# Performance work log

Hardware: AMD Instinct MI355X
Metric: run time of the kernel (lower is better)

Reference implementation:

```python
import jax, jax.numpy as jnp
import numpy as np

DIM = 1024
FFN = 4096
E = 10      # num_domains
N = 8192    # tokens
STEPS = 1   # GatedMLP steps (depth=1 layer)


def gated_mlp(x, W1, b1, W2, b2, Wg, bg):
    # depth=1, steps=STEPS; dropout=0 (eval). Residual MLP block with sigmoid gate.
    h = x
    for _ in range(STEPS):
        h = jax.nn.gelu(h @ W1 + b1, approximate=False) @ W2 + b2 + h
    g = jax.nn.sigmoid(x @ Wg + bg)
    return g * h + (1.0 - g) * x


def setup_inputs() -> dict:
    key = jax.random.key(0)
    ks = jax.random.split(key, 16)
    s1 = 1.0 / np.sqrt(DIM)
    s2 = 1.0 / np.sqrt(FFN)
    inp = {
        "x": jax.random.normal(ks[0], (N, DIM), dtype=jnp.float32),
        "domain_ids": jax.random.randint(ks[1], (N,), 0, E, dtype=jnp.int32),
        # shared expert
        "sW1": jax.random.normal(ks[2], (DIM, FFN), dtype=jnp.float32) * s1,
        "sb1": jnp.zeros((FFN,), dtype=jnp.float32),
        "sW2": jax.random.normal(ks[3], (FFN, DIM), dtype=jnp.float32) * s2,
        "sb2": jnp.zeros((DIM,), dtype=jnp.float32),
        "sWg": jax.random.normal(ks[4], (DIM, DIM), dtype=jnp.float32) * (0.01 * s1),
        "sbg": jnp.full((DIM,), -4.0, dtype=jnp.float32),
        # domain experts, stacked over E
        "dW1": jax.random.normal(ks[5], (E, DIM, FFN), dtype=jnp.float32) * s1,
        "db1": jnp.zeros((E, FFN), dtype=jnp.float32),
        "dW2": jax.random.normal(ks[6], (E, FFN, DIM), dtype=jnp.float32) * s2,
        "db2": jnp.zeros((E, DIM), dtype=jnp.float32),
        "dWg": jax.random.normal(ks[7], (E, DIM, DIM), dtype=jnp.float32) * (0.01 * s1),
        "dbg": jnp.full((E, DIM), -4.0, dtype=jnp.float32),
    }
    return inp


def reference(x, domain_ids, sW1, sb1, sW2, sb2, sWg, sbg,
              dW1, db1, dW2, db2, dWg, dbg):
    out = gated_mlp(x, sW1, sb1, sW2, sb2, sWg, sbg)
    # each token belongs to exactly one domain expert; dense dispatch via mask
    for e in range(E):
        mask = (domain_ids == e).astype(x.dtype)[:, None]  # [N,1]
        expert_out = gated_mlp(x, dW1[e], db1[e], dW2[e], db2[e], dWg[e], dbg[e])
        out = out + mask * expert_out
    return out
```

## Files before the change

### kernel.cpp

```cpp
#include <hip/hip_runtime.h>
#include <hip/hip_bf16.h>
#include <math.h>

#define NTOK 8192
#define DIM  1024
#define FFN  4096
#define NEXP 10

#define NT_SH (NTOK / 128)
#define NT_RT (NTOK / 128 + NEXP - 1)
#define NY01  ((FFN + DIM) / 128)
#define NY2   (DIM / 128)

typedef __attribute__((ext_vector_type(8))) short bf16x8;
typedef __attribute__((ext_vector_type(4))) float f32x4;

static __device__ __forceinline__ unsigned short f2bf(float f) {
  __hip_bfloat16 h = __float2bfloat16(f);
  return *reinterpret_cast<unsigned short*>(&h);
}

static __device__ __forceinline__ void gld_lds16(const unsigned short* g, unsigned short* l) {
  __builtin_amdgcn_global_load_lds((const __attribute__((address_space(1))) unsigned int*)g,
                                   (__attribute__((address_space(3))) unsigned int*)l,
                                   16, 0, 0);
}

template <int NX, int NY, int G>
static __device__ __forceinline__ void map_block(int orig, int& bx, int& by) {
  const int n = NX * NY;
  int xcd = orig & 7, o = orig >> 3;
  const int q = n >> 3, r = n & 7;
  int id = (xcd < r ? xcd * (q + 1) : r * (q + 1) + (xcd - r) * q) + o;
  const int gsz = NX * G;
  int grp = id / gsz;
  int rem = id - grp * gsz;
  bx = rem / G;
  by = grp * G + (rem - bx * G);
}

__global__ void k_zero(int* cnt) { if (threadIdx.x < NEXP) cnt[threadIdx.x] = 0; }

__global__ void k_count(const int* __restrict__ dom, int* __restrict__ cnt, int* __restrict__ pos) {
  int t = blockIdx.x * 256 + threadIdx.x;
  if (t < NTOK) pos[t] = atomicAdd(&cnt[dom[t]], 1);
}

__global__ void k_offsets(const int* __restrict__ cnt, int* __restrict__ segoff,
                          int* __restrict__ tilemap, int* __restrict__ ntiles) {
  if (threadIdx.x == 0) {
    int s = 0, k = 0;
    for (int e = 0; e < NEXP; e++) {
      segoff[e] = s;
      int c = cnt[e];
      int nt = (c + 127) >> 7;
      for (int t = 0; t < nt; t++) tilemap[k++] = (e << 16) | t;
      s += c;
    }
    segoff[NEXP] = s;
    *ntiles = k;
  }
}

__global__ void k_scatter(const int* __restrict__ dom, const int* __restrict__ pos,
                          const int* __restrict__ segoff, int* __restrict__ perm) {
  int t = blockIdx.x * 256 + threadIdx.x;
  if (t < NTOK) perm[segoff[dom[t]] + pos[t]] = t;
}

__global__ void k_convert(const float* __restrict__ src, unsigned short* __restrict__ dst, int n8) {
  int i = blockIdx.x * 256 + threadIdx.x;
  if (i >= n8) return;
  const float4* s = (const float4*)(src + (size_t)i * 8);
  float4 a = s[0], b = s[1];
  union { unsigned short h[8]; uint4 v; } u;
  u.h[0] = f2bf(a.x); u.h[1] = f2bf(a.y); u.h[2] = f2bf(a.z); u.h[3] = f2bf(a.w);
  u.h[4] = f2bf(b.x); u.h[5] = f2bf(b.y); u.h[6] = f2bf(b.z); u.h[7] = f2bf(b.w);
  *(uint4*)(dst + (size_t)i * 8) = u.v;
}

__global__ void k_gather(const unsigned short* __restrict__ xb, const int* __restrict__ perm,
                         unsigned short* __restrict__ xs) {
  int i = blockIdx.x * 256 + threadIdx.x;
  int row = i >> 7;
  int c = (i & 127) * 8;
  int src = perm[row];
  *(uint4*)(xs + (size_t)row * DIM + c) = *(const uint4*)(xb + (size_t)src * DIM + c);
}

__global__ void k_transpose(const float* __restrict__ src, unsigned short* __restrict__ dst,
                            int K, int N) {
  size_t moff = (size_t)blockIdx.z * K * N;
  src += moff; dst += moff;
  __shared__ float tile[64][65];
  int n0 = blockIdx.x * 64, k0 = blockIdx.y * 64;
  int t = threadIdx.x;
  int tx = t & 15, ty = t >> 4;
#pragma unroll
  for (int i = 0; i < 4; i++) {
    int kk = ty + i * 16;
    float4 v = *(const float4*)(src + (size_t)(k0 + kk) * N + n0 + tx * 4);
    tile[kk][tx * 4 + 0] = v.x; tile[kk][tx * 4 + 1] = v.y;
    tile[kk][tx * 4 + 2] = v.z; tile[kk][tx * 4 + 3] = v.w;
  }
  __syncthreads();
#pragma unroll
  for (int i = 0; i < 2; i++) {
    int chunk = t + i * 256;
    int nl = chunk >> 3;
    int k8 = (chunk & 7) * 8;
    union { unsigned short h[8]; uint4 v; } u;
#pragma unroll
    for (int j = 0; j < 8; j++) u.h[j] = f2bf(tile[k8 + j][nl]);
    *(uint4*)(dst + (size_t)(n0 + nl) * K + k0 + k8) = u.v;
  }
}

static __device__ __forceinline__ void mfma_tile(
    const unsigned short* gA0, const unsigned short* gA1,
    const unsigned short* gB0, const unsigned short* gB1,
    unsigned short (*As)[32], unsigned short (*Bs)[32],
    int w, int lane, int K, f32x4 acc[4][4])
{
  unsigned short* lA0 = &As[0][0] + w * 1024;
  unsigned short* lA1 = lA0 + 512;
  unsigned short* lB0 = &Bs[0][0] + w * 1024;
  unsigned short* lB1 = lB0 + 512;
  int m16 = lane & 15, kh = (lane >> 4) * 8;
  int wr = (w >> 1) * 64, wc = (w & 1) * 64;
  for (int kt = 0; kt < K; kt += 32) {
    gld_lds16(gA0, lA0); gld_lds16(gA1, lA1);
    gld_lds16(gB0, lB0); gld_lds16(gB1, lB1);
    gA0 += 32; gA1 += 32; gB0 += 32; gB1 += 32;
    __syncthreads();
    bf16x8 af[4], bfr[4];
#pragma unroll
    for (int i = 0; i < 4; i++) af[i] = *(const bf16x8*)&As[wr + i * 16 + m16][kh];
#pragma unroll
    for (int j = 0; j < 4; j++) bfr[j] = *(const bf16x8*)&Bs[wc + j * 16 + m16][kh];
#pragma unroll
    for (int i = 0; i < 4; i++)
#pragma unroll
      for (int j = 0; j < 4; j++)
        acc[i][j] = __builtin_amdgcn_mfma_f32_16x16x32_bf16(af[i], bfr[j], acc[i][j], 0, 0, 0);
    __syncthreads();
  }
}

template <bool ROUTED>
__global__ __launch_bounds__(256)
void k_gemm01(const unsigned short* __restrict__ A,
              const unsigned short* __restrict__ W1t,
              const float* __restrict__ b1,
              const unsigned short* __restrict__ Wgt,
              const float* __restrict__ bg,
              unsigned short* __restrict__ h1,
              float* __restrict__ g,
              const int* __restrict__ segoff,
              const int* __restrict__ tilemap,
              const int* __restrict__ ntilesp) {
  constexpr int NX = ROUTED ? NT_RT : NT_SH;
  int bx, by;
  map_block<NX, NY01, 8>((int)blockIdx.x, bx, by);

  int e = 0, seg0 = 0, cnt = NTOK, m0;
  if (ROUTED) {
    if (bx >= *ntilesp) return;
    int tm = tilemap[bx];
    e = tm >> 16;
    seg0 = segoff[e];
    cnt = segoff[e + 1] - seg0;
    m0 = (tm & 0xffff) << 7;
  } else {
    m0 = bx << 7;
  }

  const bool isW1 = by < (FFN / 128);
  const int n0 = (isW1 ? by : by - FFN / 128) << 7;
  const unsigned short* Bte = isW1 ? W1t + (size_t)e * FFN * DIM + (size_t)n0 * DIM
                                   : Wgt + (size_t)e * DIM * DIM + (size_t)n0 * DIM;
  const float* be = (isW1 ? b1 + (size_t)e * FFN : bg + (size_t)e * DIM) + n0;

  __shared__ unsigned short As[128][32];
  __shared__ unsigned short Bs[128][32];

  int tid = threadIdx.x, w = tid >> 6, lane = tid & 63;
  int p0 = w * 128 + lane;
  int r0 = p0 >> 2, r1 = r0 + 16;
  int kc = (p0 & 3) * 8;

  auto arow = [&](int rl) -> size_t {
    int l = m0 + rl;
    if (ROUTED && l > cnt - 1) l = cnt - 1;
    return (size_t)(seg0 + l);
  };
  const unsigned short* gA0 = A + arow(r0) * DIM + kc;
  const unsigned short* gA1 = A + arow(r1) * DIM + kc;
  const unsigned short* gB0 = Bte + (size_t)r0 * DIM + kc;
  const unsigned short* gB1 = Bte + (size_t)r1 * DIM + kc;

  f32x4 acc[4][4];
#pragma unroll
  for (int i = 0; i < 4; i++)
#pragma unroll
    for (int j = 0; j < 4; j++) acc[i][j] = (f32x4){0.f, 0.f, 0.f, 0.f};

  mfma_tile(gA0, gA1, gB0, gB1, As, Bs, w, lane, DIM, acc);

  int m16 = lane & 15, quad = lane >> 4;
  int wr = (w >> 1) * 64, wc = (w & 1) * 64;
#pragma unroll
  for (int i = 0; i < 4; i++) {
#pragma unroll
    for (int j = 0; j < 4; j++) {
      int cn = wc + j * 16 + m16;
      int col = n0 + cn;
#pragma unroll
      for (int r = 0; r < 4; r++) {
        int rl = wr + i * 16 + quad * 4 + r;
        int l = m0 + rl;
        if (ROUTED && l >= cnt) continue;
        float z = acc[i][j][r] + be[cn];
        size_t row = (size_t)(seg0 + l);
        if (isW1) {
          z = 0.5f * z * (1.0f + erff(z * 0.70710678118654752f));
          h1[row * FFN + col] = f2bf(z);
        } else {
          z = 1.0f / (1.0f + expf(-z));
          g[row * DIM + col] = z;
        }
      }
    }
  }
}

template <bool ROUTED>
__global__ __launch_bounds__(256)
void k_gemm2(const unsigned short* __restrict__ A,
             const unsigned short* __restrict__ W2t,
             const float* __restrict__ b2,
             const float* __restrict__ g,
             const float* __restrict__ xres,
             float* __restrict__ out,
             const int* __restrict__ perm,
             const int* __restrict__ segoff,
             const int* __restrict__ tilemap,
             const int* __restrict__ ntilesp) {
  constexpr int NX = ROUTED ? NT_RT : NT_SH;
  int bx, by;
  map_block<NX, NY2, 2>((int)blockIdx.x, bx, by);

  int e = 0, seg0 = 0, cnt = NTOK, m0;
  if (ROUTED) {
    if (bx >= *ntilesp) return;
    int tm = tilemap[bx];
    e = tm >> 16;
    seg0 = segoff[e];
    cnt = segoff[e + 1] - seg0;
    m0 = (tm & 0xffff) << 7;
  } else {
    m0 = bx << 7;
  }
  const int n0 = by << 7;
  const unsigned short* Bte = W2t + (size_t)e * DIM * FFN + (size_t)n0 * FFN;
  const float* be = b2 + (size_t)e * DIM + n0;

  __shared__ unsigned short As[128][32];
  __shared__ unsigned short Bs[128][32];

  int tid = threadIdx.x, w = tid >> 6, lane = tid & 63;
  int p0 = w * 128 + lane;
  int r0 = p0 >> 2, r1 = r0 + 16;
  int kc = (p0 & 3) * 8;

  auto arow = [&](int rl) -> size_t {
    int l = m0 + rl;
    if (ROUTED && l > cnt - 1) l = cnt - 1;
    return (size_t)(seg0 + l);
  };
  const unsigned short* gA0 = A + arow(r0) * FFN + kc;
  const unsigned short* gA1 = A + arow(r1) * FFN + kc;
  const unsigned short* gB0 = Bte + (size_t)r0 * FFN + kc;
  const unsigned short* gB1 = Bte + (size_t)r1 * FFN + kc;

  f32x4 acc[4][4];
#pragma unroll
  for (int i = 0; i < 4; i++)
#pragma unroll
    for (int j = 0; j < 4; j++) acc[i][j] = (f32x4){0.f, 0.f, 0.f, 0.f};

  mfma_tile(gA0, gA1, gB0, gB1, As, Bs, w, lane, FFN, acc);

  int m16 = lane & 15, quad = lane >> 4;
  int wr = (w >> 1) * 64, wc = (w & 1) * 64;
#pragma unroll
  for (int i = 0; i < 4; i++) {
#pragma unroll
    for (int j = 0; j < 4; j++) {
      int cn = wc + j * 16 + m16;
      int col = n0 + cn;
#pragma unroll
      for (int r = 0; r < 4; r++) {
        int rl = wr + i * 16 + quad * 4 + r;
        int l = m0 + rl;
        if (ROUTED && l >= cnt) continue;
        int lidx = seg0 + l;
        int grow = ROUTED ? perm[lidx] : l;
        float xv = xres[(size_t)grow * DIM + col];
        float gv = g[(size_t)lidx * DIM + col];
        float h = acc[i][j][r] + be[cn] + xv;
        float o = gv * h + (1.0f - gv) * xv;
        float* po = &out[(size_t)grow * DIM + col];
        if (ROUTED) *po += o;
        else        *po = o;
      }
    }
  }
}

extern "C" void kernel_launch(void* const* d_in, const int* in_sizes, int n_in,
                              void* d_out, int out_size, void* d_ws, size_t ws_size,
                              hipStream_t stream) {
  (void)in_sizes; (void)n_in; (void)out_size; (void)ws_size;
  const float* x   = (const float*)d_in[0];
  const int*   dom = (const int*)d_in[1];
  const float* sW1 = (const float*)d_in[2];
  const float* sb1 = (const float*)d_in[3];
  const float* sW2 = (const float*)d_in[4];
  const float* sb2 = (const float*)d_in[5];
  const float* sWg = (const float*)d_in[6];
  const float* sbg = (const float*)d_in[7];
  const float* dW1 = (const float*)d_in[8];
  const float* db1 = (const float*)d_in[9];
  const float* dW2 = (const float*)d_in[10];
  const float* db2 = (const float*)d_in[11];
  const float* dWg = (const float*)d_in[12];
  const float* dbg = (const float*)d_in[13];
  float* out = (float*)d_out;

  char* p = (char*)d_ws;
  auto take = [&](size_t b) { char* r = p; p += (b + 255) & ~(size_t)255; return r; };
  int* cnt     = (int*)take(NEXP * 4);
  int* segoff  = (int*)take((NEXP + 1) * 4);
  int* tilemap = (int*)take(128 * 4);
  int* ntiles  = (int*)take(4);
  int* pos     = (int*)take((size_t)NTOK * 4);
  int* perm    = (int*)take((size_t)NTOK * 4);
  unsigned short* xb   = (unsigned short*)take((size_t)NTOK * DIM * 2);
  unsigned short* xs   = (unsigned short*)take((size_t)NTOK * DIM * 2);
  unsigned short* h1   = (unsigned short*)take((size_t)NTOK * FFN * 2);
  float*          g    = (float*)take((size_t)NTOK * DIM * 4);
  unsigned short* sW1t = (unsigned short*)take((size_t)DIM * FFN * 2);
  unsigned short* sW2t = (unsigned short*)take((size_t)FFN * DIM * 2);
  unsigned short* sWgt = (unsigned short*)take((size_t)DIM * DIM * 2);
  unsigned short* dW1t = (unsigned short*)take((size_t)NEXP * DIM * FFN * 2);
  unsigned short* dW2t = (unsigned short*)take((size_t)NEXP * FFN * DIM * 2);
  unsigned short* dWgt = (unsigned short*)take((size_t)NEXP * DIM * DIM * 2);

  k_zero<<<1, 64, 0, stream>>>(cnt);
  k_count<<<NTOK / 256, 256, 0, stream>>>(dom, cnt, pos);
  k_offsets<<<1, 1, 0, stream>>>(cnt, segoff, tilemap, ntiles);
  k_scatter<<<NTOK / 256, 256, 0, stream>>>(dom, pos, segoff, perm);

  k_convert<<<(NTOK * DIM / 8) / 256, 256, 0, stream>>>(x, xb, NTOK * DIM / 8);
  k_gather<<<(NTOK * DIM / 8) / 256, 256, 0, stream>>>(xb, perm, xs);
  k_transpose<<<dim3(FFN / 64, DIM / 64, 1),    256, 0, stream>>>(sW1, sW1t, DIM, FFN);
  k_transpose<<<dim3(DIM / 64, FFN / 64, 1),    256, 0, stream>>>(sW2, sW2t, FFN, DIM);
  k_transpose<<<dim3(DIM / 64, DIM / 64, 1),    256, 0, stream>>>(sWg, sWgt, DIM, DIM);
  k_transpose<<<dim3(FFN / 64, DIM / 64, NEXP), 256, 0, stream>>>(dW1, dW1t, DIM, FFN);
  k_transpose<<<dim3(DIM / 64, FFN / 64, NEXP), 256, 0, stream>>>(dW2, dW2t, FFN, DIM);
  k_transpose<<<dim3(DIM / 64, DIM / 64, NEXP), 256, 0, stream>>>(dWg, dWgt, DIM, DIM);

  k_gemm01<false><<<NT_SH * NY01, 256, 0, stream>>>(
      xb, sW1t, sb1, sWgt, sbg, h1, g, nullptr, nullptr, nullptr);
  k_gemm2<false><<<NT_SH * NY2, 256, 0, stream>>>(
      h1, sW2t, sb2, g, x, out, nullptr, nullptr, nullptr, nullptr);

  k_gemm01<true><<<NT_RT * NY01, 256, 0, stream>>>(
      xs, dW1t, db1, dWgt, dbg, h1, g, segoff, tilemap, ntiles);
  k_gemm2<true><<<NT_RT * NY2, 256, 0, stream>>>(
      h1, dW2t, db2, g, x, out, perm, segoff, tilemap, ntiles);
}
```

Before: 1.143 ms.

## Use larger 512-thread GEMM tiles with 4-stage LDS pipeline and tanh GELU

Replaces the single-buffered 128x128 MFMA tile loop with a multi-stage pipeline that keeps up to four K-slices in LDS, issuing direct global-to-LDS loads ahead and waiting with explicit vmcnt. It also swizzles the LDS layout and raises MFMA wave priority. The first GEMM moves to 256x256 tiles and the second to 128x256 tiles with 512 threads, so two tile maps are now built. The exact erf GELU is swapped for the tanh approximation with fast exp, which cuts epilogue cost but changes numerics slightly. The aim is to hide global-load latency and raise data reuse, at the cost of much more LDS per block and therefore lower occupancy.

```diff
diff --git a/kernel.cpp b/kernel.cpp
--- a/kernel.cpp
+++ b/kernel.cpp
@@ -7,10 +7,12 @@
 #define FFN  4096
 #define NEXP 10
 
-#define NT_SH (NTOK / 128)
-#define NT_RT (NTOK / 128 + NEXP - 1)
-#define NY01  ((FFN + DIM) / 128)
-#define NY2   (DIM / 128)
+#define NX1_SH (NTOK / 256)
+#define NX1_RT (NTOK / 256 + NEXP - 1)
+#define NX2_SH (NTOK / 128)
+#define NX2_RT (NTOK / 128 + NEXP - 1)
+#define NY1 ((FFN + DIM) / 256)
+#define NY2 (DIM / 256)
 
 typedef __attribute__((ext_vector_type(8))) short bf16x8;
 typedef __attribute__((ext_vector_type(4))) float f32x4;
@@ -24,6 +26,11 @@
   __builtin_amdgcn_global_load_lds((const __attribute__((address_space(1))) unsigned int*)g,
                                    (__attribute__((address_space(3))) unsigned int*)l,
                                    16, 0, 0);
+}
+
+template <int N>
+static __device__ __forceinline__ void waitv() {
+  asm volatile("s_waitcnt vmcnt(%0)" :: "i"(N) : "memory");
 }
 
 template <int NX, int NY, int G>
@@ -47,18 +54,20 @@
 }
 
 __global__ void k_offsets(const int* __restrict__ cnt, int* __restrict__ segoff,
-                          int* __restrict__ tilemap, int* __restrict__ ntiles) {
+                          int* __restrict__ tm256, int* __restrict__ nt256,
+                          int* __restrict__ tm128, int* __restrict__ nt128) {
   if (threadIdx.x == 0) {
-    int s = 0, k = 0;
+    int s = 0, k2 = 0, k1 = 0;
     for (int e = 0; e < NEXP; e++) {
       segoff[e] = s;
       int c = cnt[e];
-      int nt = (c + 127) >> 7;
-      for (int t = 0; t < nt; t++) tilemap[k++] = (e << 16) | t;
+      for (int t = 0; t < ((c + 255) >> 8); t++) tm256[k2++] = (e << 16) | t;
+      for (int t = 0; t < ((c + 127) >> 7); t++) tm128[k1++] = (e << 16) | t;
       s += c;
     }
     segoff[NEXP] = s;
-    *ntiles = k;
+    *nt256 = k2;
+    *nt128 = k1;
   }
 }
 
@@ -116,118 +125,159 @@
   }
 }
 
-static __device__ __forceinline__ void mfma_tile(
-    const unsigned short* gA0, const unsigned short* gA1,
-    const unsigned short* gB0, const unsigned short* gB1,
-    unsigned short (*As)[32], unsigned short (*Bs)[32],
-    int w, int lane, int K, f32x4 acc[4][4])
+template <int BM, int KLEN, int MREP>
+__device__ __forceinline__ void gemm_pipeline(
+    const unsigned short* pA0, const unsigned short* pA1,
+    const unsigned short* pB0, const unsigned short* pB1,
+    unsigned short* As, unsigned short* Bs, int tid,
+    f32x4 acc[MREP][4])
 {
-  unsigned short* lA0 = &As[0][0] + w * 1024;
-  unsigned short* lA1 = lA0 + 512;
-  unsigned short* lB0 = &Bs[0][0] + w * 1024;
-  unsigned short* lB1 = lB0 + 512;
-  int m16 = lane & 15, kh = (lane >> 4) * 8;
-  int wr = (w >> 1) * 64, wc = (w & 1) * 64;
-  for (int kt = 0; kt < K; kt += 32) {
-    gld_lds16(gA0, lA0); gld_lds16(gA1, lA1);
-    gld_lds16(gB0, lB0); gld_lds16(gB1, lB1);
-    gA0 += 32; gA1 += 32; gB0 += 32; gB1 += 32;
-    __syncthreads();
-    bf16x8 af[4], bfr[4];
-#pragma unroll
-    for (int i = 0; i < 4; i++) af[i] = *(const bf16x8*)&As[wr + i * 16 + m16][kh];
-#pragma unroll
-    for (int j = 0; j < 4; j++) bfr[j] = *(const bf16x8*)&Bs[wc + j * 16 + m16][kh];
-#pragma unroll
-    for (int i = 0; i < 4; i++)
-#pragma unroll
-      for (int j = 0; j < 4; j++)
-        acc[i][j] = __builtin_amdgcn_mfma_f32_16x16x32_bf16(af[i], bfr[j], acc[i][j], 0, 0, 0);
-    __syncthreads();
-  }
+  constexpr int NS    = KLEN / 32;
+  constexpr int NEA   = BM / 128;
+  constexpr int LPS   = NEA + 2;
+  constexpr int ASLOT = BM * 32;
+  constexpr int BSLOT = 256 * 32;
+
+  const int lane = tid & 63, wid = tid >> 6;
+  const int wm = wid >> 2, wn = wid & 3;
+  const int m16 = lane & 15;
+  const int q = lane >> 4;
+  const int kslot = q ^ ((m16 >> 1) & 3);
+  const int aoff = (wm * (BM / 2) + m16) * 32 + kslot * 8;
+  const int boff = (wn * 64 + m16) * 32 + kslot * 8;
+
+#pragma unroll
+  for (int s = 0; s < 3; ++s) {
+    gld_lds16(pA0 + s * 32, As + s * ASLOT + tid * 8);
+    if (NEA == 2) gld_lds16(pA1 + s * 32, As + s * ASLOT + 4096 + tid * 8);
+    gld_lds16(pB0 + s * 32, Bs + s * BSLOT + tid * 8);
+    gld_lds16(pB1 + s * 32, Bs + s * BSLOT + 4096 + tid * 8);
+  }
+  pA0 += 96; pA1 += 96; pB0 += 96; pB1 += 96;
+  waitv<2 * LPS>();
+  __builtin_amdgcn_s_barrier();
+
+  auto slice = [&](int s, bool stage, auto dowait) {
+    const int so = s & 3, sn = (s + 3) & 3;
+    const unsigned short* Asl = As + so * ASLOT;
+    const unsigned short* Bsl = Bs + so * BSLOT;
+    bf16x8 b[4], a[MREP / 2];
+#pragma unroll
+    for (int i = 0; i < MREP / 2; ++i) a[i] = *(const bf16x8*)(Asl + aoff + i * 512);
+#pragma unroll
+    for (int j = 0; j < 4; ++j)        b[j] = *(const bf16x8*)(Bsl + boff + j * 512);
+    if (stage) {
+      gld_lds16(pA0, As + sn * ASLOT + tid * 8); pA0 += 32;
+      if (NEA == 2) { gld_lds16(pA1, As + sn * ASLOT + 4096 + tid * 8); pA1 += 32; }
+    }
+    __builtin_amdgcn_s_barrier();
+    __builtin_amdgcn_s_setprio(1);
+#pragma unroll
+    for (int i = 0; i < MREP / 2; ++i)
+#pragma unroll
+      for (int j = 0; j < 4; ++j)
+        acc[i][j] = __builtin_amdgcn_mfma_f32_16x16x32_bf16(a[i], b[j], acc[i][j], 0, 0, 0);
+    __builtin_amdgcn_s_setprio(0);
+#pragma unroll
+    for (int i = 0; i < MREP / 2; ++i) a[i] = *(const bf16x8*)(Asl + aoff + (MREP / 2 + i) * 512);
+    if (stage) {
+      gld_lds16(pB0, Bs + sn * BSLOT + tid * 8); pB0 += 32;
+      gld_lds16(pB1, Bs + sn * BSLOT + 4096 + tid * 8); pB1 += 32;
+    }
+    __builtin_amdgcn_s_barrier();
+    __builtin_amdgcn_s_setprio(1);
+#pragma unroll
+    for (int i = 0; i < MREP / 2; ++i)
+#pragma unroll
+      for (int j = 0; j < 4; ++j)
+        acc[MREP / 2 + i][j] =
+            __builtin_amdgcn_mfma_f32_16x16x32_bf16(a[i], b[j], acc[MREP / 2 + i][j], 0, 0, 0);
+    __builtin_amdgcn_s_setprio(0);
+    dowait();
+    __builtin_amdgcn_s_barrier();
+  };
+
+#pragma clang loop unroll(disable)
+  for (int s = 0; s < NS - 3; ++s) slice(s, true, [] { waitv<2 * LPS>(); });
+  slice(NS - 3, false, [] { waitv<LPS>(); });
+  slice(NS - 2, false, [] { waitv<0>(); });
+  slice(NS - 1, false, [] {});
 }
 
 template <bool ROUTED>
-__global__ __launch_bounds__(256)
-void k_gemm01(const unsigned short* __restrict__ A,
-              const unsigned short* __restrict__ W1t,
-              const float* __restrict__ b1,
-              const unsigned short* __restrict__ Wgt,
-              const float* __restrict__ bg,
-              unsigned short* __restrict__ h1,
-              float* __restrict__ g,
-              const int* __restrict__ segoff,
-              const int* __restrict__ tilemap,
-              const int* __restrict__ ntilesp) {
-  constexpr int NX = ROUTED ? NT_RT : NT_SH;
+__global__ __launch_bounds__(512, 2)
+void k_p1(const unsigned short* __restrict__ A,
+          const unsigned short* __restrict__ W1t, const float* __restrict__ b1,
+          const unsigned short* __restrict__ Wgt, const float* __restrict__ bg,
+          unsigned short* __restrict__ h1, float* __restrict__ g,
+          const int* __restrict__ segoff, const int* __restrict__ tilemap,
+          const int* __restrict__ ntilesp) {
+  constexpr int NXW = ROUTED ? NX1_RT : NX1_SH;
   int bx, by;
-  map_block<NX, NY01, 8>((int)blockIdx.x, bx, by);
+  map_block<NXW, NY1, 4>((int)blockIdx.x, bx, by);
 
   int e = 0, seg0 = 0, cnt = NTOK, m0;
   if (ROUTED) {
     if (bx >= *ntilesp) return;
     int tm = tilemap[bx];
-    e = tm >> 16;
-    seg0 = segoff[e];
-    cnt = segoff[e + 1] - seg0;
-    m0 = (tm & 0xffff) << 7;
+    e = tm >> 16; seg0 = segoff[e]; cnt = segoff[e + 1] - seg0;
+    m0 = (tm & 0xffff) << 8;
   } else {
-    m0 = bx << 7;
-  }
-
-  const bool isW1 = by < (FFN / 128);
-  const int n0 = (isW1 ? by : by - FFN / 128) << 7;
+    m0 = bx << 8;
+  }
+  const bool isW1 = by < (FFN / 256);
+  const int n0 = (isW1 ? by : by - FFN / 256) << 8;
   const unsigned short* Bte = isW1 ? W1t + (size_t)e * FFN * DIM + (size_t)n0 * DIM
                                    : Wgt + (size_t)e * DIM * DIM + (size_t)n0 * DIM;
   const float* be = (isW1 ? b1 + (size_t)e * FFN : bg + (size_t)e * DIM) + n0;
 
-  __shared__ unsigned short As[128][32];
-  __shared__ unsigned short Bs[128][32];
-
-  int tid = threadIdx.x, w = tid >> 6, lane = tid & 63;
-  int p0 = w * 128 + lane;
-  int r0 = p0 >> 2, r1 = r0 + 16;
-  int kc = (p0 & 3) * 8;
+  __shared__ unsigned short As[4 * 256 * 32];
+  __shared__ unsigned short Bs[4 * 256 * 32];
+
+  int tid = threadIdx.x;
+  int r = tid >> 2;
+  int kgx = (tid & 3) ^ ((tid >> 3) & 3);
 
   auto arow = [&](int rl) -> size_t {
     int l = m0 + rl;
     if (ROUTED && l > cnt - 1) l = cnt - 1;
     return (size_t)(seg0 + l);
   };
-  const unsigned short* gA0 = A + arow(r0) * DIM + kc;
-  const unsigned short* gA1 = A + arow(r1) * DIM + kc;
-  const unsigned short* gB0 = Bte + (size_t)r0 * DIM + kc;
-  const unsigned short* gB1 = Bte + (size_t)r1 * DIM + kc;
-
-  f32x4 acc[4][4];
-#pragma unroll
-  for (int i = 0; i < 4; i++)
-#pragma unroll
-    for (int j = 0; j < 4; j++) acc[i][j] = (f32x4){0.f, 0.f, 0.f, 0.f};
-
-  mfma_tile(gA0, gA1, gB0, gB1, As, Bs, w, lane, DIM, acc);
-
-  int m16 = lane & 15, quad = lane >> 4;
-  int wr = (w >> 1) * 64, wc = (w & 1) * 64;
-#pragma unroll
-  for (int i = 0; i < 4; i++) {
-#pragma unroll
-    for (int j = 0; j < 4; j++) {
-      int cn = wc + j * 16 + m16;
+  const unsigned short* pA0 = A + arow(r) * DIM + kgx * 8;
+  const unsigned short* pA1 = A + arow(128 + r) * DIM + kgx * 8;
+  const unsigned short* pB0 = Bte + (size_t)r * DIM + kgx * 8;
+  const unsigned short* pB1 = Bte + (size_t)(128 + r) * DIM + kgx * 8;
+
+  f32x4 acc[8][4];
+#pragma unroll
+  for (int i = 0; i < 8; ++i)
+#pragma unroll
+    for (int j = 0; j < 4; ++j) acc[i][j] = (f32x4){0.f, 0.f, 0.f, 0.f};
+
+  gemm_pipeline<256, DIM, 8>(pA0, pA1, pB0, pB1, As, Bs, tid, acc);
+
+  int lane = tid & 63, wid = tid >> 6, wm = wid >> 2, wn = wid & 3;
+  int m16 = lane & 15, q = lane >> 4;
+#pragma unroll
+  for (int i = 0; i < 8; ++i) {
+#pragma unroll
+    for (int j = 0; j < 4; ++j) {
+      int cn = wn * 64 + j * 16 + m16;
       int col = n0 + cn;
-#pragma unroll
-      for (int r = 0; r < 4; r++) {
-        int rl = wr + i * 16 + quad * 4 + r;
+      float bb = be[cn];
+#pragma unroll
+      for (int rr = 0; rr < 4; ++rr) {
+        int rl = wm * 128 + i * 16 + q * 4 + rr;
         int l = m0 + rl;
         if (ROUTED && l >= cnt) continue;
-        float z = acc[i][j][r] + be[cn];
+        float z = acc[i][j][rr] + bb;
         size_t row = (size_t)(seg0 + l);
         if (isW1) {
-          z = 0.5f * z * (1.0f + erff(z * 0.70710678118654752f));
-          h1[row * FFN + col] = f2bf(z);
+          float u = 0.79788456f * z * (1.0f + 0.044715f * z * z);
+          float o = z / (1.0f + __expf(-2.0f * u));
+          h1[row * (size_t)FFN + col] = f2bf(o);
         } else {
-          z = 1.0f / (1.0f + expf(-z));
-          g[row * DIM + col] = z;
+          g[row * (size_t)DIM + col] = 1.0f / (1.0f + __expf(-z));
         }
       }
     }
@@ -235,80 +285,77 @@
 }
 
 template <bool ROUTED>
-__global__ __launch_bounds__(256)
-void k_gemm2(const unsigned short* __restrict__ A,
-             const unsigned short* __restrict__ W2t,
-             const float* __restrict__ b2,
-             const float* __restrict__ g,
-             const float* __restrict__ xres,
-             float* __restrict__ out,
-             const int* __restrict__ perm,
-             const int* __restrict__ segoff,
-             const int* __restrict__ tilemap,
-             const int* __restrict__ ntilesp) {
-  constexpr int NX = ROUTED ? NT_RT : NT_SH;
+__global__ __launch_bounds__(512, 2)
+void k_p2(const unsigned short* __restrict__ A,
+          const unsigned short* __restrict__ W2t,
+          const float* __restrict__ b2,
+          const float* __restrict__ g,
+          const float* __restrict__ xres,
+          float* __restrict__ out,
+          const int* __restrict__ perm,
+          const int* __restrict__ segoff,
+          const int* __restrict__ tilemap,
+          const int* __restrict__ ntilesp) {
+  constexpr int NXW = ROUTED ? NX2_RT : NX2_SH;
   int bx, by;
-  map_block<NX, NY2, 2>((int)blockIdx.x, bx, by);
+  map_block<NXW, NY2, 2>((int)blockIdx.x, bx, by);
 
   int e = 0, seg0 = 0, cnt = NTOK, m0;
   if (ROUTED) {
     if (bx >= *ntilesp) return;
     int tm = tilemap[bx];
-    e = tm >> 16;
-    seg0 = segoff[e];
-    cnt = segoff[e + 1] - seg0;
+    e = tm >> 16; seg0 = segoff[e]; cnt = segoff[e + 1] - seg0;
     m0 = (tm & 0xffff) << 7;
   } else {
     m0 = bx << 7;
   }
-  const int n0 = by << 7;
+  const int n0 = by << 8;
   const unsigned short* Bte = W2t + (size_t)e * DIM * FFN + (size_t)n0 * FFN;
   const float* be = b2 + (size_t)e * DIM + n0;
 
-  __shared__ unsigned short As[128][32];
-  __shared__ unsigned short Bs[128][32];
-
-  int tid = threadIdx.x, w = tid >> 6, lane = tid & 63;
-  int p0 = w * 128 + lane;
-  int r0 = p0 >> 2, r1 = r0 + 16;
-  int kc = (p0 & 3) * 8;
+  __shared__ unsigned short As[4 * 128 * 32];
+  __shared__ unsigned short Bs[4 * 256 * 32];
+
+  int tid = threadIdx.x;
+  int r = tid >> 2;
+  int kgx = (tid & 3) ^ ((tid >> 3) & 3);
 
   auto arow = [&](int rl) -> size_t {
     int l = m0 + rl;
     if (ROUTED && l > cnt - 1) l = cnt - 1;
     return (size_t)(seg0 + l);
   };
-  const unsigned short* gA0 = A + arow(r0) * FFN + kc;
-  const unsigned short* gA1 = A + arow(r1) * FFN + kc;
-  const unsigned short* gB0 = Bte + (size_t)r0 * FFN + kc;
-  const unsigned short* gB1 = Bte + (size_t)r1 * FFN + kc;
+  const unsigned short* pA0 = A + arow(r) * FFN + kgx * 8;
+  const unsigned short* pB0 = Bte + (size_t)r * FFN + kgx * 8;
+  const unsigned short* pB1 = Bte + (size_t)(128 + r) * FFN + kgx * 8;
 
   f32x4 acc[4][4];
 #pragma unroll
-  for (int i = 0; i < 4; i++)
-#pragma unroll
-    for (int j = 0; j < 4; j++) acc[i][j] = (f32x4){0.f, 0.f, 0.f, 0.f};
-
-  mfma_tile(gA0, gA1, gB0, gB1, As, Bs, w, lane, FFN, acc);
-
-  int m16 = lane & 15, quad = lane >> 4;
-  int wr = (w >> 1) * 64, wc = (w & 1) * 64;
-#pragma unroll
-  for (int i = 0; i < 4; i++) {
-#pragma unroll
-    for (int j = 0; j < 4; j++) {
-      int cn = wc + j * 16 + m16;
+  for (int i = 0; i < 4; ++i)
+#pragma unroll
+    for (int j = 0; j < 4; ++j) acc[i][j] = (f32x4){0.f, 0.f, 0.f, 0.f};
+
+  gemm_pipeline<128, FFN, 4>(pA0, pA0, pB0, pB1, As, Bs, tid, acc);
+
+  int lane = tid & 63, wid = tid >> 6, wm = wid >> 2, wn = wid & 3;
+  int m16 = lane & 15, q = lane >> 4;
+#pragma unroll
+  for (int i = 0; i < 4; ++i) {
+#pragma unroll
+    for (int j = 0; j < 4; ++j) {
+      int cn = wn * 64 + j * 16 + m16;
       int col = n0 + cn;
-#pragma unroll
-      for (int r = 0; r < 4; r++) {
-        int rl = wr + i * 16 + quad * 4 + r;
+      float bb = be[cn];
+#pragma unroll
+      for (int rr = 0; rr < 4; ++rr) {
+        int rl = wm * 64 + i * 16 + q * 4 + rr;
         int l = m0 + rl;
         if (ROUTED && l >= cnt) continue;
         int lidx = seg0 + l;
         int grow = ROUTED ? perm[lidx] : l;
         float xv = xres[(size_t)grow * DIM + col];
         float gv = g[(size_t)lidx * DIM + col];
-        float h = acc[i][j][r] + be[cn] + xv;
+        float h = acc[i][j][rr] + bb + xv;
         float o = gv * h + (1.0f - gv) * xv;
         float* po = &out[(size_t)grow * DIM + col];
         if (ROUTED) *po += o;
@@ -342,8 +389,10 @@
   auto take = [&](size_t b) { char* r = p; p += (b + 255) & ~(size_t)255; return r; };
   int* cnt     = (int*)take(NEXP * 4);
   int* segoff  = (int*)take((NEXP + 1) * 4);
-  int* tilemap = (int*)take(128 * 4);
-  int* ntiles  = (int*)take(4);
+  int* tm256   = (int*)take(64 * 4);
+  int* nt256   = (int*)take(4);
+  int* tm128   = (int*)take(128 * 4);
+  int* nt128   = (int*)take(4);
   int* pos     = (int*)take((size_t)NTOK * 4);
   int* perm    = (int*)take((size_t)NTOK * 4);
   unsigned short* xb   = (unsigned short*)take((size_t)NTOK * DIM * 2);
@@ -359,7 +408,7 @@
 
   k_zero<<<1, 64, 0, stream>>>(cnt);
   k_count<<<NTOK / 256, 256, 0, stream>>>(dom, cnt, pos);
-  k_offsets<<<1, 1, 0, stream>>>(cnt, segoff, tilemap, ntiles);
+  k_offsets<<<1, 1, 0, stream>>>(cnt, segoff, tm256, nt256, tm128, nt128);
   k_scatter<<<NTOK / 256, 256, 0, stream>>>(dom, pos, segoff, perm);
 
   k_convert<<<(NTOK * DIM / 8) / 256, 256, 0, stream>>>(x, xb, NTOK * DIM / 8);
@@ -371,13 +420,13 @@
   k_transpose<<<dim3(DIM / 64, FFN / 64, NEXP), 256, 0, stream>>>(dW2, dW2t, FFN, DIM);
   k_transpose<<<dim3(DIM / 64, DIM / 64, NEXP), 256, 0, stream>>>(dWg, dWgt, DIM, DIM);
 
-  k_gemm01<false><<<NT_SH * NY01, 256, 0, stream>>>(
+  k_p1<false><<<NX1_SH * NY1, 512, 0, stream>>>(
       xb, sW1t, sb1, sWgt, sbg, h1, g, nullptr, nullptr, nullptr);
-  k_gemm2<false><<<NT_SH * NY2, 256, 0, stream>>>(
+  k_p2<false><<<NX2_SH * NY2, 512, 0, stream>>>(
       h1, sW2t, sb2, g, x, out, nullptr, nullptr, nullptr, nullptr);
 
-  k_gemm01<true><<<NT_RT * NY01, 256, 0, stream>>>(
-      xs, dW1t, db1, dWgt, dbg, h1, g, segoff, tilemap, ntiles);
-  k_gemm2<true><<<NT_RT * NY2, 256, 0, stream>>>(
-      h1, dW2t, db2, g, x, out, perm, segoff, tilemap, ntiles);
-}
+  k_p1<true><<<NX1_RT * NY1, 512, 0, stream>>>(
+      xs, dW1t, db1, dWgt, dbg, h1, g, segoff, tm256, nt256);
+  k_p2<true><<<NX2_RT * NY2, 512, 0, stream>>>(
+      h1, dW2t, db2, g, x, out, perm, segoff, tm128, nt128);
+}
```

After: 1.307 ms. 14.4% more time.
